# Kernel tuning notes

Measured on AMD Instinct MI355X. Metric: run time of the kernel, lower is better.

Reference implementation:

```python
import jax, jax.numpy as jnp
import numpy as np

MAX_LAG_FRACTION = 0.25
EPS = 1e-8
B, T = 1024, 2048


def setup_inputs() -> dict:
    key = jax.random.key(0)
    k1, k2, k3 = jax.random.split(key, 3)
    alpha_pred = jax.random.uniform(k1, (B,), dtype=jnp.float32)          # alpha in [0,1)
    D0_pred = jax.random.uniform(k2, (B,), dtype=jnp.float32)             # D0 in [0,1)
    trajectory = jax.random.normal(k3, (B, T, 2), dtype=jnp.float32)
    return {"alpha_pred": alpha_pred, "D0_pred": D0_pred, "trajectory": trajectory}


def _msd_all_lags(traj, max_lag):
    # traj: (B, T, C). Returns empirical MSD per sample per lag: (B, max_lag).
    Bn, Tn, _ = traj.shape
    t = jnp.arange(Tn)

    def step(carry, lag):
        idx = jnp.clip(t + lag, 0, Tn - 1)                    # (T,)
        disp = jnp.take(traj, idx, axis=1) - traj             # (B, T, C)
        sq = jnp.sum(disp * disp, axis=-1)                    # (B, T) squared displacement
        valid = (t + lag < Tn).astype(sq.dtype)               # (T,) mask for t in [0, T-lag)
        msd = jnp.sum(sq * valid[None, :], axis=-1) / jnp.maximum(jnp.sum(valid), 1.0)
        return carry, msd                                      # (B,)

    lags = jnp.arange(1, max_lag + 1)
    _, msd = jax.lax.scan(step, None, lags)                   # (max_lag, B)
    return msd.T                                               # (B, max_lag)


def reference(alpha_pred, D0_pred, trajectory):
    Bn, Tn, _ = trajectory.shape
    max_lag = max(1, int(Tn * MAX_LAG_FRACTION))
    msd_emp = _msd_all_lags(trajectory, max_lag)                               # (B, L)
    lags = jnp.arange(1, max_lag + 1, dtype=trajectory.dtype)                  # (L,)
    msd_theo = 4.0 * D0_pred[:, None] * jnp.power(lags[None, :], alpha_pred[:, None])  # (B, L)
    d = jnp.log(msd_theo + EPS) - jnp.log(msd_emp + EPS)
    # per-sample MSE over lags, then mean over batch (same as original loop)
    return jnp.mean(jnp.mean(d * d, axis=-1))
```

## Files before the change

### kernel.cpp

```cpp
#include <hip/hip_runtime.h>

#define B_SAMPLES 1024
#define T_LEN     2048
#define NLAG      512
#define ROWW      172

typedef _Float16 half8_t __attribute__((ext_vector_type(8)));
typedef float    floatx4 __attribute__((ext_vector_type(4)));

__device__ __forceinline__ int slotP(int k) { return k + (k >> 5); }

__global__ __launch_bounds__(256) void msd_mfma_kernel(
    const float* __restrict__ alpha, const float* __restrict__ d0p,
    const float* __restrict__ traj, float* __restrict__ partial) {
  const int b   = blockIdx.x;
  const int tid = threadIdx.x;
  const int w   = tid >> 6;
  const int l   = tid & 63;
  const int g   = l >> 4;
  const int p16 = l & 15;

  __shared__ __align__(16) unsigned int Zw[16 * ROWW];
  __shared__ float Pb[2116];
  __shared__ float Elds[33][16];
  __shared__ float cT[4];
  __shared__ float wred[4];

  for (int k = tid; k < 16 * 44; k += 256)
    Zw[(k / 44) * ROWW + 128 + (k % 44)] = 0u;

  const float4* tr4 = reinterpret_cast<const float4*>(traj) + (size_t)b * (T_LEN / 2);
  float sq[8];
  #pragma unroll
  for (int s = 0; s < 4; ++s) {
    int idx = (w << 8) + (l << 2) + s;
    float4 v4 = tr4[idx];
    int t0 = idx << 1;
    _Float16 hx0 = (_Float16)v4.x, hy0 = (_Float16)v4.y;
    _Float16 hx1 = (_Float16)v4.z, hy1 = (_Float16)v4.w;
    unsigned int wd0 = (unsigned int)__builtin_bit_cast(unsigned short, hx0)
                     | ((unsigned int)__builtin_bit_cast(unsigned short, hy0) << 16);
    unsigned int wd1 = (unsigned int)__builtin_bit_cast(unsigned short, hx1)
                     | ((unsigned int)__builtin_bit_cast(unsigned short, hy1) << 16);
    Zw[(t0 & 15) * ROWW + (t0 >> 4)] = wd0;
    Zw[((t0 + 1) & 15) * ROWW + ((t0 + 1) >> 4)] = wd1;
    float fx0 = (float)hx0, fy0 = (float)hy0;
    float fx1 = (float)hx1, fy1 = (float)hy1;
    sq[2 * s]     = fmaf(fx0, fx0, fy0 * fy0);
    sq[2 * s + 1] = fmaf(fx1, fx1, fy1 * fy1);
  }

  float ls = ((sq[0] + sq[1]) + (sq[2] + sq[3])) + ((sq[4] + sq[5]) + (sq[6] + sq[7]));
  float run = ls;
  #pragma unroll
  for (int dlt = 1; dlt < 64; dlt <<= 1) {
    float tsh = __shfl_up(run, dlt, 64);
    if (l >= dlt) run += tsh;
  }
  float excl = run - ls;
  if (l == 63) cT[w] = run;

  __syncthreads();

  float c0 = cT[0], c1 = cT[1], c2 = cT[2], c3 = cT[3];
  const float Ptot = (c0 + c1) + (c2 + c3);
  float off = 0.f;
  if (w > 0) off += c0;
  if (w > 1) off += c1;
  if (w > 2) off += c2;
  float r2 = off + excl;
  #pragma unroll
  for (int i = 0; i < 8; ++i) {
    r2 += sq[i];
    Pb[slotP((w << 9) + (l << 3) + i + 1)] = r2;
  }

  const unsigned int* zrow = &Zw[p16 * ROWW];
  const int vS = 8 * w;

  floatx4 D[9];
  #pragma unroll
  for (int r = 0; r < 9; ++r) D[r] = (floatx4){0.f, 0.f, 0.f, 0.f};

  #pragma unroll
  for (int q = 0; q < 8; ++q) {
    const unsigned int* wp = zrow + 16 * q + 4 * g + vS;
    uint4 w0 = *reinterpret_cast<const uint4*>(wp);
    uint4 w1 = *reinterpret_cast<const uint4*>(wp + 4);
    uint4 w2 = *reinterpret_cast<const uint4*>(wp + 8);
    unsigned int win[12] = {w0.x, w0.y, w0.z, w0.w,  w1.x, w1.y, w1.z, w1.w,
                            w2.x, w2.y, w2.z, w2.w};
    uint4 aw = *reinterpret_cast<const uint4*>(zrow + 16 * q + 4 * g);
    half8_t aq = __builtin_bit_cast(half8_t, aw);
    #pragma unroll
    for (int r = 0; r < 9; ++r) {
      uint4 bw;
      bw.x = win[r]; bw.y = win[r + 1]; bw.z = win[r + 2]; bw.w = win[r + 3];
      half8_t bf = __builtin_bit_cast(half8_t, bw);
      D[r] = __builtin_amdgcn_mfma_f32_16x16x32_f16(aq, bf, D[r], 0, 0, 0);
    }
  }

  float prevA = 0.f;
  const int rotb = 4 * g + p16;
  const int idx0 = (l & 48) << 2;

  #pragma unroll
  for (int r = 0; r < 9; ++r) {
    float accA = 0.f, accB = 0.f;
    #pragma unroll
    for (int rr = 0; rr < 4; ++rr) {
      float gv = D[r][rr];
      int src = idx0 | (((rotb + rr) & 15) << 2);
      float got = __builtin_bit_cast(float,
          __builtin_amdgcn_ds_bpermute(src, __builtin_bit_cast(int, gv)));
      bool wrap = (rotb + rr) >= 16;
      accA += wrap ? 0.f : got;
      accB += wrap ? got : 0.f;
    }
    if (r > 0) {
      float E = prevA + accB;
      E += __shfl_xor(E, 16, 64);
      E += __shfl_xor(E, 32, 64);
      if (l < 16) Elds[vS + r - 1][p16] = E;
    }
    prevA = accA;
  }
  if (w == 3) {
    float E = prevA;
    E += __shfl_xor(E, 16, 64);
    E += __shfl_xor(E, 32, 64);
    if (l == 0) Elds[32][0] = E;
  }
  __syncthreads();

  const float aexp = alpha[b];
  const float c4d0 = 4.f * d0p[b];
  float loc = 0.f;
  #pragma unroll
  for (int c = 0; c < 2; ++c) {
    int lag = c * 256 + tid + 1;
    float E  = Elds[lag >> 4][lag & 15];
    float Pl = Pb[slotP(lag)];
    int mm   = 2048 - lag;
    float Pr = Pb[slotP(mm)];
    float S2  = Pr + (Ptot - Pl);
    float msd = fmaxf((S2 - 2.f * E) / (float)mm, 0.f);
    float theo = c4d0 * __builtin_exp2f(aexp * __builtin_log2f((float)lag));
    float dd = 0.69314718f * (__builtin_log2f(theo + 1e-8f) - __builtin_log2f(msd + 1e-8f));
    loc = fmaf(dd, dd, loc);
  }

  #pragma unroll
  for (int dlt = 1; dlt < 64; dlt <<= 1) loc += __shfl_xor(loc, dlt, 64);
  if (l == 0) wred[w] = loc;
  __syncthreads();
  if (tid == 0) partial[b] = (wred[0] + wred[1]) + (wred[2] + wred[3]);
}

__global__ __launch_bounds__(256) void reduce_kernel(
    const float* __restrict__ partial, float* __restrict__ out) {
  __shared__ float wsum[4];
  float acc = 0.f;
  for (int i = threadIdx.x; i < B_SAMPLES; i += 256) acc += partial[i];
  for (int off = 32; off > 0; off >>= 1) acc += __shfl_down(acc, off, 64);
  const int wid  = threadIdx.x >> 6;
  const int lane = threadIdx.x & 63;
  if (lane == 0) wsum[wid] = acc;
  __syncthreads();
  if (threadIdx.x == 0) {
    float t = wsum[0] + wsum[1] + wsum[2] + wsum[3];
    out[0] = t * (1.0f / ((float)B_SAMPLES * (float)NLAG));
  }
}

extern "C" void kernel_launch(void* const* d_in, const int* in_sizes, int n_in,
                              void* d_out, int out_size, void* d_ws, size_t ws_size,
                              hipStream_t stream) {
  const float* alpha = (const float*)d_in[0];
  const float* d0p   = (const float*)d_in[1];
  const float* traj  = (const float*)d_in[2];
  float* out     = (float*)d_out;
  float* partial = (float*)d_ws;

  msd_mfma_kernel<<<B_SAMPLES, 256, 0, stream>>>(alpha, d0p, traj, partial);
  reduce_kernel<<<1, 256, 0, stream>>>(partial, out);
}
```

Baseline: 16.33 us.

## Split each sample's lag range across two blocks to double grid parallelism

Launches two blocks per sample, each computing the MFMA autocorrelation for half of the lag range (5 accumulator tiles instead of 9). Each block still loads the whole trajectory and builds the full prefix sums, so the load and prefix work is duplicated. The reduce kernel now sums 2048 partials. The aim is more blocks for occupancy and shorter per-block critical paths, at the cost of redundant global loads and LDS setup.

```diff
diff --git a/kernel.cpp b/kernel.cpp
--- a/kernel.cpp
+++ b/kernel.cpp
@@ -13,7 +13,9 @@
 __global__ __launch_bounds__(256) void msd_mfma_kernel(
     const float* __restrict__ alpha, const float* __restrict__ d0p,
     const float* __restrict__ traj, float* __restrict__ partial) {
-  const int b   = blockIdx.x;
+  const int bb  = blockIdx.x;
+  const int b   = bb >> 1;
+  const int h   = bb & 1;
   const int tid = threadIdx.x;
   const int w   = tid >> 6;
   const int l   = tid & 63;
@@ -22,7 +24,7 @@
 
   __shared__ __align__(16) unsigned int Zw[16 * ROWW];
   __shared__ float Pb[2116];
-  __shared__ float Elds[33][16];
+  __shared__ float Elds[17][16];
   __shared__ float cT[4];
   __shared__ float wred[4];
 
@@ -69,6 +71,7 @@
   if (w > 1) off += c1;
   if (w > 2) off += c2;
   float r2 = off + excl;
+  if (tid == 0) Pb[0] = 0.f;
   #pragma unroll
   for (int i = 0; i < 8; ++i) {
     r2 += sq[i];
@@ -76,24 +79,22 @@
   }
 
   const unsigned int* zrow = &Zw[p16 * ROWW];
-  const int vS = 8 * w;
-
-  floatx4 D[9];
-  #pragma unroll
-  for (int r = 0; r < 9; ++r) D[r] = (floatx4){0.f, 0.f, 0.f, 0.f};
+  const int vS = 16 * h + 4 * w;
+
+  floatx4 D[5];
+  #pragma unroll
+  for (int r = 0; r < 5; ++r) D[r] = (floatx4){0.f, 0.f, 0.f, 0.f};
 
   #pragma unroll
   for (int q = 0; q < 8; ++q) {
     const unsigned int* wp = zrow + 16 * q + 4 * g + vS;
     uint4 w0 = *reinterpret_cast<const uint4*>(wp);
     uint4 w1 = *reinterpret_cast<const uint4*>(wp + 4);
-    uint4 w2 = *reinterpret_cast<const uint4*>(wp + 8);
-    unsigned int win[12] = {w0.x, w0.y, w0.z, w0.w,  w1.x, w1.y, w1.z, w1.w,
-                            w2.x, w2.y, w2.z, w2.w};
+    unsigned int win[8] = {w0.x, w0.y, w0.z, w0.w,  w1.x, w1.y, w1.z, w1.w};
     uint4 aw = *reinterpret_cast<const uint4*>(zrow + 16 * q + 4 * g);
     half8_t aq = __builtin_bit_cast(half8_t, aw);
     #pragma unroll
-    for (int r = 0; r < 9; ++r) {
+    for (int r = 0; r < 5; ++r) {
       uint4 bw;
       bw.x = win[r]; bw.y = win[r + 1]; bw.z = win[r + 2]; bw.w = win[r + 3];
       half8_t bf = __builtin_bit_cast(half8_t, bw);
@@ -106,7 +107,7 @@
   const int idx0 = (l & 48) << 2;
 
   #pragma unroll
-  for (int r = 0; r < 9; ++r) {
+  for (int r = 0; r < 5; ++r) {
     float accA = 0.f, accB = 0.f;
     #pragma unroll
     for (int rr = 0; rr < 4; ++rr) {
@@ -122,47 +123,72 @@
       float E = prevA + accB;
       E += __shfl_xor(E, 16, 64);
       E += __shfl_xor(E, 32, 64);
-      if (l < 16) Elds[vS + r - 1][p16] = E;
+      if (l < 16) Elds[4 * w + r - 1][p16] = E;
     }
     prevA = accA;
   }
-  if (w == 3) {
+  if (h == 1 && w == 3) {
     float E = prevA;
     E += __shfl_xor(E, 16, 64);
     E += __shfl_xor(E, 32, 64);
-    if (l == 0) Elds[32][0] = E;
+    if (l == 0) Elds[16][0] = E;
   }
   __syncthreads();
 
   const float aexp = alpha[b];
   const float c4d0 = 4.f * d0p[b];
   float loc = 0.f;
-  #pragma unroll
-  for (int c = 0; c < 2; ++c) {
-    int lag = c * 256 + tid + 1;
-    float E  = Elds[lag >> 4][lag & 15];
-    float Pl = Pb[slotP(lag)];
-    int mm   = 2048 - lag;
-    float Pr = Pb[slotP(mm)];
-    float S2  = Pr + (Ptot - Pl);
-    float msd = fmaxf((S2 - 2.f * E) / (float)mm, 0.f);
-    float theo = c4d0 * __builtin_exp2f(aexp * __builtin_log2f((float)lag));
-    float dd = 0.69314718f * (__builtin_log2f(theo + 1e-8f) - __builtin_log2f(msd + 1e-8f));
-    loc = fmaf(dd, dd, loc);
+
+  if (h == 0) {
+    if (tid < 255) {
+      int lag = tid + 1;
+      float E  = Elds[lag >> 4][lag & 15];
+      float Pl = Pb[slotP(lag)];
+      int mm   = 2048 - lag;
+      float Pr = Pb[slotP(mm)];
+      float S2  = Pr + (Ptot - Pl);
+      float msd = fmaxf((S2 - 2.f * E) / (float)mm, 0.f);
+      float theo = c4d0 * __builtin_exp2f(aexp * __builtin_log2f((float)lag));
+      float dd = 0.69314718f * (__builtin_log2f(theo + 1e-8f) - __builtin_log2f(msd + 1e-8f));
+      loc = dd * dd;
+    }
+  } else {
+    {
+      int lag = 256 + tid;
+      float E  = Elds[(lag >> 4) - 16][lag & 15];
+      float Pl = Pb[slotP(lag)];
+      int mm   = 2048 - lag;
+      float Pr = Pb[slotP(mm)];
+      float S2  = Pr + (Ptot - Pl);
+      float msd = fmaxf((S2 - 2.f * E) / (float)mm, 0.f);
+      float theo = c4d0 * __builtin_exp2f(aexp * __builtin_log2f((float)lag));
+      float dd = 0.69314718f * (__builtin_log2f(theo + 1e-8f) - __builtin_log2f(msd + 1e-8f));
+      loc = dd * dd;
+    }
+    if (tid == 255) {
+      float E  = Elds[16][0];
+      float Pl = Pb[slotP(512)];
+      float Pr = Pb[slotP(1536)];
+      float S2  = Pr + (Ptot - Pl);
+      float msd = fmaxf((S2 - 2.f * E) * (1.f / 1536.f), 0.f);
+      float theo = c4d0 * __builtin_exp2f(aexp * __builtin_log2f(512.f));
+      float dd = 0.69314718f * (__builtin_log2f(theo + 1e-8f) - __builtin_log2f(msd + 1e-8f));
+      loc += dd * dd;
+    }
   }
 
   #pragma unroll
   for (int dlt = 1; dlt < 64; dlt <<= 1) loc += __shfl_xor(loc, dlt, 64);
   if (l == 0) wred[w] = loc;
   __syncthreads();
-  if (tid == 0) partial[b] = (wred[0] + wred[1]) + (wred[2] + wred[3]);
+  if (tid == 0) partial[bb] = (wred[0] + wred[1]) + (wred[2] + wred[3]);
 }
 
 __global__ __launch_bounds__(256) void reduce_kernel(
     const float* __restrict__ partial, float* __restrict__ out) {
   __shared__ float wsum[4];
   float acc = 0.f;
-  for (int i = threadIdx.x; i < B_SAMPLES; i += 256) acc += partial[i];
+  for (int i = threadIdx.x; i < 2 * B_SAMPLES; i += 256) acc += partial[i];
   for (int off = 32; off > 0; off >>= 1) acc += __shfl_down(acc, off, 64);
   const int wid  = threadIdx.x >> 6;
   const int lane = threadIdx.x & 63;
@@ -183,6 +209,6 @@
   float* out     = (float*)d_out;
   float* partial = (float*)d_ws;
 
-  msd_mfma_kernel<<<B_SAMPLES, 256, 0, stream>>>(alpha, d0p, traj, partial);
+  msd_mfma_kernel<<<2 * B_SAMPLES, 256, 0, stream>>>(alpha, d0p, traj, partial);
   reduce_kernel<<<1, 256, 0, stream>>>(partial, out);
 }
```

Result: slower. 18.18 us (+11.3%).

## Pack MFMA outputs into fp16 pairs for bpermute and skip unused prefix stores

Applied to the files above, without the earlier changes.

Pairs of fp32 MFMA accumulator rows are packed into half2 words with cvt_pkrtz before the ds_bpermute rotation and the xor-shuffle reductions. This roughly halves the cross-lane permute and shuffle traffic in the epilogue. Separately, the prefix-sum buffer is written only for the index ranges the lag loop actually reads (first and last quarters plus one boundary value), which removes most LDS stores. The cost is reduced precision in the cross-correlation terms, which are rounded to fp16 before subtraction from the squared-sum terms.

```diff
diff --git a/kernel.cpp b/kernel.cpp
--- a/kernel.cpp
+++ b/kernel.cpp
@@ -5,6 +5,7 @@
 #define NLAG      512
 #define ROWW      172
 
+typedef __fp16   half2_t __attribute__((ext_vector_type(2)));
 typedef _Float16 half8_t __attribute__((ext_vector_type(8)));
 typedef float    floatx4 __attribute__((ext_vector_type(4)));
 
@@ -69,10 +70,16 @@
   if (w > 1) off += c1;
   if (w > 2) off += c2;
   float r2 = off + excl;
-  #pragma unroll
-  for (int i = 0; i < 8; ++i) {
-    r2 += sq[i];
-    Pb[slotP((w << 9) + (l << 3) + i + 1)] = r2;
+  if (w == 0 || w == 3) {
+    #pragma unroll
+    for (int i = 0; i < 8; ++i) {
+      r2 += sq[i];
+      Pb[slotP((w << 9) + (l << 3) + i + 1)] = r2;
+    }
+  } else if (w == 2 && l == 63) {
+    float r3 = r2 + ((sq[0] + sq[1]) + (sq[2] + sq[3])) +
+               ((sq[4] + sq[5]) + (sq[6] + sq[7]));
+    Pb[slotP(1536)] = r3;
   }
 
   const unsigned int* zrow = &Zw[p16 * ROWW];
@@ -101,33 +108,54 @@
     }
   }
 
-  float prevA = 0.f;
+  float accA[9], accB[9];
+  #pragma unroll
+  for (int r = 0; r < 9; ++r) { accA[r] = 0.f; accB[r] = 0.f; }
+
   const int rotb = 4 * g + p16;
   const int idx0 = (l & 48) << 2;
 
   #pragma unroll
-  for (int r = 0; r < 9; ++r) {
-    float accA = 0.f, accB = 0.f;
+  for (int rr = 0; rr < 4; ++rr) {
+    const int src  = idx0 | (((rotb + rr) & 15) << 2);
+    const bool wrap = (rotb + rr) >= 16;
     #pragma unroll
-    for (int rr = 0; rr < 4; ++rr) {
-      float gv = D[r][rr];
-      int src = idx0 | (((rotb + rr) & 15) << 2);
-      float got = __builtin_bit_cast(float,
-          __builtin_amdgcn_ds_bpermute(src, __builtin_bit_cast(int, gv)));
-      bool wrap = (rotb + rr) >= 16;
-      accA += wrap ? 0.f : got;
-      accB += wrap ? got : 0.f;
-    }
-    if (r > 0) {
-      float E = prevA + accB;
-      E += __shfl_xor(E, 16, 64);
-      E += __shfl_xor(E, 32, 64);
-      if (l < 16) Elds[vS + r - 1][p16] = E;
-    }
-    prevA = accA;
+    for (int pr = 0; pr < 4; ++pr) {
+      half2_t pk = __builtin_amdgcn_cvt_pkrtz(D[2 * pr][rr], D[2 * pr + 1][rr]);
+      int got = __builtin_amdgcn_ds_bpermute(src, __builtin_bit_cast(int, pk));
+      half2_t gh = __builtin_bit_cast(half2_t, got);
+      float lo = (float)gh[0], hi = (float)gh[1];
+      accA[2 * pr]     += wrap ? 0.f : lo;
+      accB[2 * pr]     += wrap ? lo : 0.f;
+      accA[2 * pr + 1] += wrap ? 0.f : hi;
+      accB[2 * pr + 1] += wrap ? hi : 0.f;
+    }
+    {
+      int got = __builtin_amdgcn_ds_bpermute(src, __builtin_bit_cast(int, D[8][rr]));
+      float gv = __builtin_bit_cast(float, got);
+      accA[8] += wrap ? 0.f : gv;
+      accB[8] += wrap ? gv : 0.f;
+    }
+  }
+
+  #pragma unroll
+  for (int k = 0; k < 4; ++k) {
+    float e0 = accA[2 * k]     + accB[2 * k + 1];
+    float e1 = accA[2 * k + 1] + accB[2 * k + 2];
+    half2_t pk = __builtin_amdgcn_cvt_pkrtz(e0, e1);
+    half2_t t1 = __builtin_bit_cast(half2_t,
+        __shfl_xor(__builtin_bit_cast(int, pk), 16, 64));
+    pk = pk + t1;
+    half2_t t2 = __builtin_bit_cast(half2_t,
+        __shfl_xor(__builtin_bit_cast(int, pk), 32, 64));
+    pk = pk + t2;
+    if (l < 16) {
+      Elds[vS + 2 * k][p16]     = (float)pk[0];
+      Elds[vS + 2 * k + 1][p16] = (float)pk[1];
+    }
   }
   if (w == 3) {
-    float E = prevA;
+    float E = accA[8];
     E += __shfl_xor(E, 16, 64);
     E += __shfl_xor(E, 32, 64);
     if (l == 0) Elds[32][0] = E;
```

New measurement: 16.31 us. Within noise of the previous version (-0.1%).
